# Performance work log

Hardware: AMD Instinct MI355X
Metric: run time of the kernel (lower is better)

Reference implementation:

```python
import jax, jax.numpy as jnp
import numpy as np
from jax import lax

TAG_NUM = 20
START = TAG_NUM - 2  # tag2idx[START_TAG]
STOP = TAG_NUM - 1   # tag2idx[STOP_TAG]
NEG = -10000.0


def setup_inputs() -> dict:
    key = jax.random.key(0)
    k1, k2, k3, k4 = jax.random.split(key, 4)
    B, L = 256, 512
    feats = jax.random.normal(k1, (B, L, TAG_NUM), dtype=jnp.float32)
    T = jax.random.normal(k2, (TAG_NUM, TAG_NUM), dtype=jnp.float32)
    # transitions into START and out of... match torch init: T[START, :] = -1e4 ; T[:, STOP] = -1e4
    T = T.at[START, :].set(NEG).at[:, STOP].set(NEG)
    tags = jax.random.randint(k3, (B, L), 0, TAG_NUM - 2, dtype=jnp.int64)  # real tags only
    lengths = jax.random.randint(k4, (B,), 1, L + 1, dtype=jnp.int64)
    return {"feats": feats, "T": T, "tags": tags, "lengths": lengths}


def crf_neg_log_likelihood(feats, T, tags, lengths):
    # feats: [B, L, tag], T: [tag, tag] (T[i, j] = score of transition i -> j)
    B, L, tg = feats.shape
    mask = jnp.arange(L)[None, :] < lengths[:, None]           # [B, L] bool
    # scores[b, l, prev, cur] = feats[b, l, cur] + T[prev, cur]
    scores = feats[:, :, None, :] + T[None, None, :, :]        # [B, L, tag, tag]
    scores_lb = jnp.swapaxes(scores, 0, 1)                     # [L, B, tag, tag]
    mask_lb = mask.T                                           # [L, B]

    # ---- forward algorithm (log partition) ----
    part0 = scores_lb[0, :, START, :]                          # [B, tag]
    def step(part, x):
        sc, m = x                                              # sc: [B, tag, tag], m: [B]
        cur = jax.nn.logsumexp(sc + part[:, :, None], axis=1)  # [B, tag]
        part = jnp.where(m[:, None], cur, part)                # freeze past seq end
        return part, None
    part, _ = lax.scan(step, part0, (scores_lb[1:], mask_lb[1:]))
    final = jax.nn.logsumexp(part[:, :, None] + T[None, :, :], axis=1)  # [B, tag]
    forward_score = final[:, STOP].sum()

    # ---- gold score ----
    prev = jnp.concatenate([jnp.full((B, 1), START, dtype=tags.dtype), tags[:, :-1]], axis=1)
    b_idx = jnp.arange(B)[:, None]
    l_idx = jnp.arange(L)[None, :]
    tg_energy = scores[b_idx, l_idx, prev, tags]               # [B, L]
    gold = jnp.sum(tg_energy * mask.astype(feats.dtype))
    end_ids = jnp.take_along_axis(tags, lengths[:, None] - 1, axis=1)[:, 0]
    gold = gold + T[end_ids, STOP].sum()

    return forward_score - gold


def reference(feats, T, tags, lengths):
    return crf_neg_log_likelihood(feats, T, tags, lengths)
```

## Files before the change

### kernel.cpp

```cpp
#include <hip/hip_runtime.h>
#include <hip/hip_bf16.h>
#include <math.h>

#define TAGS   20
#define TSTART (TAGS - 2)
#define TSTOP  (TAGS - 1)

constexpr float  LOG2E = 1.4426950408889634f;
constexpr float  LN2f  = 0.6931471805599453f;
constexpr double LN2d  = 0.69314718055994530942;

typedef __attribute__((ext_vector_type(8))) short short8;
typedef __attribute__((ext_vector_type(4))) float f32x4;
union U4 { unsigned int u[4]; short8 v; };

__device__ __forceinline__ unsigned int pk2(float lo, float hi) {
    unsigned int a = __float_as_uint(hi) + 0x8000u;
    unsigned int b = __float_as_uint(lo) + 0x8000u;
#if __has_builtin(__builtin_amdgcn_perm)
    return __builtin_amdgcn_perm(a, b, 0x07060302u);
#else
    return (a & 0xFFFF0000u) | (b >> 16);
#endif
}
__device__ __forceinline__ float fexp2(float x) { return exp2f(x); }
__device__ __forceinline__ float flog2(float x) { return log2f(x); }
__device__ __forceinline__ float frcp(float x) { return __builtin_amdgcn_rcpf(x); }
__device__ __forceinline__ float bcast(float v, int srclane) {
    return __int_as_float(__builtin_amdgcn_readlane(__float_as_int(v), srclane));
}
__device__ __forceinline__ int rho(int k) {
    int g = k >> 3, i = k & 7;
    return (i < 4) ? (4 * g + i) : (16 + 4 * g + (i - 4));
}

__global__ __launch_bounds__(512)
void crf_fused_kernel(const float* __restrict__ feats,
                      const float* __restrict__ Tm,
                      const int*   __restrict__ tags,
                      const int*   __restrict__ lengths,
                      double*      __restrict__ partial,
                      int L)
{
    __shared__ float  smem[16 * 1024];
    __shared__ float  sv[32];
    __shared__ int    EsX[8];
    __shared__ float  gred[8];
    __shared__ double fwd_sh;

    const int b    = blockIdx.x;
    const int tid  = threadIdx.x;
    const int w    = tid >> 6;
    const int lane = tid & 63;
    const int G    = lane >> 4, col = lane & 15;
    const int len  = lengths[b];

    #pragma unroll
    for (int s = 0; s < 2; ++s) {
        const int c = w + 8 * s;
        float* efc = smem + c * 1024;
        const float* fc = feats + ((size_t)b * L + (size_t)c * 32) * TAGS;
        for (int it = lane; it < 160; it += 64) {
            float4 v = reinterpret_cast<const float4*>(fc)[it];
            float vv[4] = {v.x, v.y, v.z, v.w};
            #pragma unroll
            for (int u = 0; u < 4; ++u) {
                int f = it * 4 + u;
                int t = f / TAGS, tag = f - t * TAGS;
                efc[t * 32 + tag] = fexp2(vv[u] * LOG2E);
            }
        }
        for (int q = lane; q < 32 * 12; q += 64) {
            int t = q / 12;
            efc[t * 32 + 20 + (q - t * 12)] = 0.f;
        }
    }
    __syncthreads();

    U4 A0, A1;
    #pragma unroll
    for (int t = 0; t < 4; ++t) {
        int k0 = 8 * G + 2 * t;
        int r0 = rho(k0), r1 = rho(k0 + 1);
        int m1 = 16 + col;
        float a00 = (r0 < TAGS) ? fexp2(Tm[col * TAGS + r0] * LOG2E) : 0.f;
        float a01 = (r1 < TAGS) ? fexp2(Tm[col * TAGS + r1] * LOG2E) : 0.f;
        float a10 = (m1 < TAGS && r0 < TAGS) ? fexp2(Tm[m1 * TAGS + r0] * LOG2E) : 0.f;
        float a11 = (m1 < TAGS && r1 < TAGS) ? fexp2(Tm[m1 * TAGS + r1] * LOG2E) : 0.f;
        A0.u[t] = pk2(a00, a01);
        A1.u[t] = pk2(a10, a11);
    }

    auto step = [&](f32x4& C00, f32x4& C01, f32x4& C10, f32x4& C11,
                    const float* efc, int t) {
        float4 e0 = *reinterpret_cast<const float4*>(&efc[t * 32 + 4 * G]);
        float4 e1 = *reinterpret_cast<const float4*>(&efc[t * 32 + 16 + 4 * G]);
        U4 B0, B1;
        B0.u[0] = pk2(C00[0] * e0.x, C00[1] * e0.y);
        B0.u[1] = pk2(C00[2] * e0.z, C00[3] * e0.w);
        B0.u[2] = pk2(C10[0] * e1.x, C10[1] * e1.y);
        B0.u[3] = pk2(C10[2] * e1.z, C10[3] * e1.w);
        B1.u[0] = pk2(C01[0] * e0.x, C01[1] * e0.y);
        B1.u[1] = pk2(C01[2] * e0.z, C01[3] * e0.w);
        B1.u[2] = pk2(C11[0] * e1.x, C11[1] * e1.y);
        B1.u[3] = pk2(C11[2] * e1.z, C11[3] * e1.w);
        f32x4 z = {0.f, 0.f, 0.f, 0.f};
        C00 = __builtin_amdgcn_mfma_f32_16x16x32_bf16(A0.v, B0.v, z, 0, 0, 0);
        C01 = __builtin_amdgcn_mfma_f32_16x16x32_bf16(A0.v, B1.v, z, 0, 0, 0);
        C10 = __builtin_amdgcn_mfma_f32_16x16x32_bf16(A1.v, B0.v, z, 0, 0, 0);
        C11 = __builtin_amdgcn_mfma_f32_16x16x32_bf16(A1.v, B1.v, z, 0, 0, 0);
    };
    auto strip = [&](f32x4& C00, f32x4& C01, f32x4& C10, f32x4& C11) -> int {
        float pr = C00[0] + C00[1] + C00[2] + C00[3] + C10[0] + C10[1] + C10[2] + C10[3];
        int pb = __builtin_amdgcn_readfirstlane(__float_as_int(pr));
        int ex = ((pb >> 23) & 0xFF) - 127;
        float s = __uint_as_float((unsigned)(127 - ex) << 23);
        #pragma unroll
        for (int j = 0; j < 4; ++j) { C00[j] *= s; C01[j] *= s; C10[j] *= s; C11[j] *= s; }
        return ex;
    };
    auto xwr = [&](int slot, const f32x4& C00, const f32x4& C01,
                   const f32x4& C10, const f32x4& C11, int E) {
        float* Xs = smem + slot * 1088;
        #pragma unroll
        for (int j = 0; j < 4; ++j) {
            Xs[(4 * G + j) * 34 + col]           = C00[j];
            Xs[(4 * G + j) * 34 + col + 16]      = C01[j];
            Xs[(16 + 4 * G + j) * 34 + col]      = C10[j];
            Xs[(16 + 4 * G + j) * 34 + col + 16] = C11[j];
        }
        if (lane == 0) EsX[slot] = E;
    };
    auto prod = [&](int slot, f32x4& C00, f32x4& C01, f32x4& C10, f32x4& C11) -> int {
        const float* Xs = smem + slot * 1088;
        U4 Ax0, Ax1;
        #pragma unroll
        for (int t = 0; t < 4; ++t) {
            int r = rho(8 * G + 2 * t);
            float2 x0 = *reinterpret_cast<const float2*>(&Xs[col * 34 + r]);
            float2 x1 = *reinterpret_cast<const float2*>(&Xs[(16 + col) * 34 + r]);
            Ax0.u[t] = pk2(x0.x, x0.y);
            Ax1.u[t] = pk2(x1.x, x1.y);
        }
        U4 B0, B1;
        B0.u[0] = pk2(C00[0], C00[1]);
        B0.u[1] = pk2(C00[2], C00[3]);
        B0.u[2] = pk2(C10[0], C10[1]);
        B0.u[3] = pk2(C10[2], C10[3]);
        B1.u[0] = pk2(C01[0], C01[1]);
        B1.u[1] = pk2(C01[2], C01[3]);
        B1.u[2] = pk2(C11[0], C11[1]);
        B1.u[3] = pk2(C11[2], C11[3]);
        f32x4 z = {0.f, 0.f, 0.f, 0.f};
        f32x4 n00 = __builtin_amdgcn_mfma_f32_16x16x32_bf16(Ax0.v, B0.v, z, 0, 0, 0);
        f32x4 n01 = __builtin_amdgcn_mfma_f32_16x16x32_bf16(Ax0.v, B1.v, z, 0, 0, 0);
        f32x4 n10 = __builtin_amdgcn_mfma_f32_16x16x32_bf16(Ax1.v, B0.v, z, 0, 0, 0);
        f32x4 n11 = __builtin_amdgcn_mfma_f32_16x16x32_bf16(Ax1.v, B1.v, z, 0, 0, 0);
        C00 = n00; C01 = n01; C10 = n10; C11 = n11;
        return strip(C00, C01, C10, C11);
    };

    f32x4 aC00, aC01, aC10, aC11, bC00, bC01, bC10, bC11;
    #pragma unroll
    for (int j = 0; j < 4; ++j) {
        float d = (4 * G + j == col) ? 1.f : 0.f;
        aC00[j] = d; aC11[j] = d; aC01[j] = 0.f; aC10[j] = 0.f;
        bC00[j] = d; bC11[j] = d; bC01[j] = 0.f; bC10[j] = 0.f;
    }
    int aE = 0, bE = 0;

    const int cB  = w + 8;
    const int loA = (w == 0) ? 1 : w * 32;
    const int hiA = min(w * 32 + 31, len - 1);
    const int loB = cB * 32;
    const int hiB = min(cB * 32 + 31, len - 1);
    int nA = hiA - loA + 1; if (nA < 0) nA = 0;
    int nB = hiB - loB + 1; if (nB < 0) nB = 0;
    const int n = max(nA, nB);
    const float* efA = smem + w * 1024;
    const float* efB = smem + cB * 1024;

    int lA = hiA, lB = hiB;
    for (int i = 0; i < n; ++i) {
        if (i < nA) { step(aC00, aC01, aC10, aC11, efA, lA - w * 32);  --lA; }
        if (i < nB) { step(bC00, bC01, bC10, bC11, efB, lB - cB * 32); --lB; }
        if ((i & 3) == 3) {
            aE += strip(aC00, aC01, aC10, aC11);
            bE += strip(bC00, bC01, bC10, bC11);
        }
    }
    __syncthreads();

    if ((w & 1) == 0) {
        xwr(w / 2,     aC00, aC01, aC10, aC11, aE);
        xwr(w / 2 + 4, bC00, bC01, bC10, bC11, bE);
    }
    __syncthreads();
    if (w & 1) {
        int pA = (w - 1) / 2;
        aE += EsX[pA]     + prod(pA,     aC00, aC01, aC10, aC11);
        bE += EsX[pA + 4] + prod(pA + 4, bC00, bC01, bC10, bC11);
    }
    __syncthreads();
    if (w == 1 || w == 5) {
        xwr((w - 1) / 4,     aC00, aC01, aC10, aC11, aE);
        xwr((w - 1) / 4 + 2, bC00, bC01, bC10, bC11, bE);
    }
    __syncthreads();
    if (w == 3 || w == 7) {
        int q = (w - 3) / 4;
        aE += EsX[q]     + prod(q,     aC00, aC01, aC10, aC11);
        bE += EsX[q + 2] + prod(q + 2, bC00, bC01, bC10, bC11);
    }
    __syncthreads();
    if (w == 3) {
        xwr(0, aC00, aC01, aC10, aC11, aE);
        xwr(1, bC00, bC01, bC10, bC11, bE);
    }
    __syncthreads();
    if (w == 7) {
        aE += EsX[0] + prod(0, aC00, aC01, aC10, aC11);
        bE += EsX[1] + prod(1, bC00, bC01, bC10, bC11);
    }
    __syncthreads();
    if (w == 7) {
        xwr(0, aC00, aC01, aC10, aC11, aE);
        int ex = prod(0, bC00, bC01, bC10, bC11);
        int fE = aE + bE + ex;
        float* Gt = smem;
        #pragma unroll
        for (int j = 0; j < 4; ++j) {
            Gt[col * 34 + 4 * G + j]            = bC00[j];
            Gt[col * 34 + 16 + 4 * G + j]       = bC10[j];
            Gt[(col + 16) * 34 + 4 * G + j]     = bC01[j];
            Gt[(col + 16) * 34 + 16 + 4 * G + j]= bC11[j];
        }
        if (lane == 0) EsX[0] = fE;
    }
    __syncthreads();

    if (w == 0) {
        const int n2 = lane & 31;
        float p = (n2 < TAGS) ? (feats[(size_t)b * L * TAGS + n2] + Tm[TSTART * TAGS + n2]) * LOG2E
                              : -1e30f;
        float mx = p;
        #pragma unroll
        for (int off = 32; off; off >>= 1) mx = fmaxf(mx, __shfl_xor(mx, off));
        float v = (n2 < TAGS) ? fexp2(p - mx) : 0.f;
        if (lane < 32) sv[lane] = v;
        const float* Gt = smem;
        float vn = 0.f;
        #pragma unroll
        for (int r = 0; r < 32; r += 2) {
            float2 g2 = *reinterpret_cast<const float2*>(&Gt[n2 * 34 + r]);
            vn = fmaf(sv[r], g2.x, vn);
            vn = fmaf(sv[r + 1], g2.y, vn);
        }
        float cstop = Tm[n2 * TAGS + TSTOP];
        float mc = (n2 < TAGS) ? cstop : -INFINITY;
        #pragma unroll
        for (int off = 32; off; off >>= 1) mc = fmaxf(mc, __shfl_xor(mc, off));
        float ts = (lane < 32 && n2 < TAGS) ? vn * fexp2((cstop - mc) * LOG2E) : 0.f;
        #pragma unroll
        for (int off = 32; off; off >>= 1) ts += __shfl_xor(ts, off);
        if (lane == 0)
            fwd_sh = ((double)mx + (double)EsX[0] + (double)flog2(ts)) * LN2d + (double)mc;
    }

    float g = 0.f;
    for (int l = tid; l < len; l += 512) {
        int tt = tags[(size_t)b * L + l];
        int pv = (l == 0) ? TSTART : tags[(size_t)b * L + l - 1];
        g += feats[((size_t)b * L + l) * TAGS + tt] + Tm[pv * TAGS + tt];
    }
    #pragma unroll
    for (int off = 32; off; off >>= 1) g += __shfl_xor(g, off);
    if (lane == 0) gred[w] = g;
    __syncthreads();

    if (tid == 0) {
        float gs = gred[0] + gred[1] + gred[2] + gred[3]
                 + gred[4] + gred[5] + gred[6] + gred[7];
        double gold = (double)gs + (double)Tm[tags[(size_t)b * L + len - 1] * TAGS + TSTOP];
        partial[b] = fwd_sh - gold;
    }
}

__global__ __launch_bounds__(64)
void crf_fwd_kernel(const float* __restrict__ feats,
                    const float* __restrict__ Tm,
                    const int*   __restrict__ tags,
                    const int*   __restrict__ lengths,
                    double*      __restrict__ partial,
                    int B, int L)
{
    __shared__ float le[512 * TAGS];
    const int b    = blockIdx.x;
    const int lane = threadIdx.x;
    const int j    = (lane < TAGS) ? lane : 0;
    const float* fb  = feats + (size_t)b * L * TAGS;
    const int*   tg  = tags  + (size_t)b * L;
    const int    len = lengths[b];

    const int nv4 = (L * TAGS) >> 2;
    for (int it = lane; it < nv4; it += 64) {
        float4 v = reinterpret_cast<const float4*>(fb)[it];
        float4 e;
        e.x = fexp2(v.x * LOG2E); e.y = fexp2(v.y * LOG2E);
        e.z = fexp2(v.z * LOG2E); e.w = fexp2(v.w * LOG2E);
        reinterpret_cast<float4*>(le)[it] = e;
    }
    __syncthreads();

    float ET[TAGS];
    #pragma unroll
    for (int i = 0; i < TAGS; ++i) ET[i] = fexp2(Tm[i * TAGS + j] * LOG2E);

    float w0   = flog2(le[j]) + Tm[TSTART * TAGS + j] * LOG2E;
    float base = bcast(w0, 0);
    float P    = fexp2(w0 - base);
    float M2   = base;
    float Pa[TAGS];
    #pragma unroll
    for (int i = 0; i < TAGS; ++i) Pa[i] = bcast(P, i);
    const float* leb = le + j;

    auto STEP = [&](int l, float efv, float rsv, bool scaled) {
        float s0 = 0.f, s1 = 0.f, s2 = 0.f, s3 = 0.f;
        #pragma unroll
        for (int i = 0; i < TAGS; i += 4) {
            s0 = fmaf(ET[i + 0], Pa[i + 0], s0);
            s1 = fmaf(ET[i + 1], Pa[i + 1], s1);
            s2 = fmaf(ET[i + 2], Pa[i + 2], s2);
            s3 = fmaf(ET[i + 3], Pa[i + 3], s3);
        }
        float s   = (s0 + s1) + (s2 + s3);
        float cur = s * efv;
        float pn  = (l < len) ? cur : P;
        P = scaled ? pn * rsv : pn;
        #pragma unroll
        for (int i = 0; i < TAGS; ++i) Pa[i] = bcast(P, i);
    };

    float efb[4];
    #pragma unroll
    for (int k = 0; k < 4; ++k) { int ln = 1 + k; ln = (ln < L) ? ln : (L - 1); efb[k] = leb[ln * TAGS]; }

    float rs = 1.0f, lg0 = 0.0f;
    int l0 = 1;
    for (; l0 + 3 < L; l0 += 4) {
        if (l0 >= len) break;
        float efn[4];
        #pragma unroll
        for (int k = 0; k < 4; ++k) { int ln = l0 + 4 + k; ln = (ln < L) ? ln : (L - 1); efn[k] = leb[ln * TAGS]; }
        M2 += lg0;
        STEP(l0 + 0, efb[0], rs, true);
        STEP(l0 + 1, efb[1], 1.f, false);
        STEP(l0 + 2, efb[2], 1.f, false);
        STEP(l0 + 3, efb[3], 1.f, false);
        float p0 = Pa[0];
        rs = frcp(p0); lg0 = flog2(p0);
        #pragma unroll
        for (int k = 0; k < 4; ++k) efb[k] = efn[k];
    }
    if (l0 < len) {
        int rem = L - l0;
        M2 += lg0;
        if (rem > 0) STEP(l0 + 0, efb[0], rs, true);
        if (rem > 1) STEP(l0 + 1, efb[1], 1.f, false);
        if (rem > 2) STEP(l0 + 2, efb[2], 1.f, false);
        if (rem > 3) STEP(l0 + 3, efb[3], 1.f, false);
    }

    float cstop = Tm[j * TAGS + TSTOP];
    float mc = (lane < TAGS) ? cstop : -INFINITY;
    #pragma unroll
    for (int off = 32; off; off >>= 1) mc = fmaxf(mc, __shfl_xor(mc, off));
    float t = (lane < TAGS) ? P * fexp2((cstop - mc) * LOG2E) : 0.f;
    #pragma unroll
    for (int off = 32; off; off >>= 1) t += __shfl_xor(t, off);
    double fwd = ((double)M2 + (double)flog2(t)) * LN2d + (double)mc;

    float g = 0.f;
    for (int l = lane; l < len; l += 64) {
        int tt = tg[l];
        int pv = (l == 0) ? TSTART : tg[l - 1];
        g += flog2(le[l * TAGS + tt]) * LN2f + Tm[pv * TAGS + tt];
    }
    #pragma unroll
    for (int off = 32; off; off >>= 1) g += __shfl_xor(g, off);

    if (lane == 0) {
        double gold = (double)g + (double)Tm[tg[len - 1] * TAGS + TSTOP];
        partial[b] = fwd - gold;
    }
}

__global__ __launch_bounds__(256)
void crf_reduce_kernel(const double* __restrict__ partial, float* __restrict__ out, int B)
{
    __shared__ double sh[256];
    const int t = threadIdx.x;
    double acc = 0.0;
    for (int i = t; i < B; i += 256) acc += partial[i];
    sh[t] = acc;
    __syncthreads();
    for (int s = 128; s; s >>= 1) {
        if (t < s) sh[t] += sh[t + s];
        __syncthreads();
    }
    if (t == 0) out[0] = (float)sh[0];
}

extern "C" void kernel_launch(void* const* d_in, const int* in_sizes, int n_in,
                              void* d_out, int out_size, void* d_ws, size_t ws_size,
                              hipStream_t stream)
{
    const float* feats   = (const float*)d_in[0];
    const float* Tm      = (const float*)d_in[1];
    const int*   tags    = (const int*)d_in[2];
    const int*   lengths = (const int*)d_in[3];

    const int B = in_sizes[3];
    const int L = in_sizes[2] / B;

    double* partial = (double*)d_ws;

    if (L == 512 && ws_size >= (size_t)B * sizeof(double)) {
        crf_fused_kernel<<<B, 512, 0, stream>>>(feats, Tm, tags, lengths, partial, L);
        crf_reduce_kernel<<<1, 256, 0, stream>>>(partial, (float*)d_out, B);
    } else {
        crf_fwd_kernel<<<B, 64, 0, stream>>>(feats, Tm, tags, lengths, partial, B, L);
        crf_reduce_kernel<<<1, 256, 0, stream>>>(partial, (float*)d_out, B);
    }
}
```

Before: 28.87 us.

## Switch CRF chunk matmuls from four 16x16 MFMAs to two chained 32x32 MFMAs

Replaces the four 16x16x32 bf16 MFMAs per step (a 2x2 tiling of the 32x32 transition product) with two accumulating 32x32x16 bf16 MFMAs, which changes the register layout of the running product and every shared-memory write and read in the tree reduction. It also swaps exp2f/log2f for the raw hardware intrinsics and removes the __syncthreads between the feature preload and the transition-matrix setup. The aim is fewer MFMA issues and less packing work on the serial dependency chain. The risks are the longer latency of the chained 32x32 MFMA, and a possible race now that the barrier is gone, if no later barrier comes before the loop reads the preloaded features.

```diff
diff --git a/kernel.cpp b/kernel.cpp
--- a/kernel.cpp
+++ b/kernel.cpp
@@ -10,8 +10,8 @@
 constexpr float  LN2f  = 0.6931471805599453f;
 constexpr double LN2d  = 0.69314718055994530942;
 
-typedef __attribute__((ext_vector_type(8))) short short8;
-typedef __attribute__((ext_vector_type(4))) float f32x4;
+typedef __attribute__((ext_vector_type(8)))  short short8;
+typedef __attribute__((ext_vector_type(16))) float f32x16;
 union U4 { unsigned int u[4]; short8 v; };
 
 __device__ __forceinline__ unsigned int pk2(float lo, float hi) {
@@ -23,15 +23,26 @@
     return (a & 0xFFFF0000u) | (b >> 16);
 #endif
 }
+#if __has_builtin(__builtin_amdgcn_exp2f)
+__device__ __forceinline__ float fexp2(float x) { return __builtin_amdgcn_exp2f(x); }
+#else
 __device__ __forceinline__ float fexp2(float x) { return exp2f(x); }
+#endif
+#if __has_builtin(__builtin_amdgcn_logf)
+__device__ __forceinline__ float flog2(float x) { return __builtin_amdgcn_logf(x); }
+#else
 __device__ __forceinline__ float flog2(float x) { return log2f(x); }
+#endif
 __device__ __forceinline__ float frcp(float x) { return __builtin_amdgcn_rcpf(x); }
 __device__ __forceinline__ float bcast(float v, int srclane) {
     return __int_as_float(__builtin_amdgcn_readlane(__float_as_int(v), srclane));
 }
-__device__ __forceinline__ int rho(int k) {
-    int g = k >> 3, i = k & 7;
-    return (i < 4) ? (4 * g + i) : (16 + 4 * g + (i - 4));
+
+__device__ __forceinline__ int kbase(int p, int h) {
+    return (p < 2) ? (4 * h + 2 * p) : (8 + 4 * h + 2 * (p - 2));
+}
+__device__ __forceinline__ int crow(int j, int h) {
+    return (j & 3) + 8 * (j >> 2) + 4 * h;
 }
 
 __global__ __launch_bounds__(512)
@@ -52,7 +63,8 @@
     const int tid  = threadIdx.x;
     const int w    = tid >> 6;
     const int lane = tid & 63;
-    const int G    = lane >> 4, col = lane & 15;
+    const int m    = lane & 31;
+    const int h    = lane >> 5;
     const int len  = lengths[b];
 
     #pragma unroll
@@ -75,97 +87,88 @@
             efc[t * 32 + 20 + (q - t * 12)] = 0.f;
         }
     }
-    __syncthreads();
-
-    U4 A0, A1;
-    #pragma unroll
-    for (int t = 0; t < 4; ++t) {
-        int k0 = 8 * G + 2 * t;
-        int r0 = rho(k0), r1 = rho(k0 + 1);
-        int m1 = 16 + col;
-        float a00 = (r0 < TAGS) ? fexp2(Tm[col * TAGS + r0] * LOG2E) : 0.f;
-        float a01 = (r1 < TAGS) ? fexp2(Tm[col * TAGS + r1] * LOG2E) : 0.f;
-        float a10 = (m1 < TAGS && r0 < TAGS) ? fexp2(Tm[m1 * TAGS + r0] * LOG2E) : 0.f;
-        float a11 = (m1 < TAGS && r1 < TAGS) ? fexp2(Tm[m1 * TAGS + r1] * LOG2E) : 0.f;
-        A0.u[t] = pk2(a00, a01);
-        A1.u[t] = pk2(a10, a11);
-    }
-
-    auto step = [&](f32x4& C00, f32x4& C01, f32x4& C10, f32x4& C11,
-                    const float* efc, int t) {
-        float4 e0 = *reinterpret_cast<const float4*>(&efc[t * 32 + 4 * G]);
-        float4 e1 = *reinterpret_cast<const float4*>(&efc[t * 32 + 16 + 4 * G]);
-        U4 B0, B1;
-        B0.u[0] = pk2(C00[0] * e0.x, C00[1] * e0.y);
-        B0.u[1] = pk2(C00[2] * e0.z, C00[3] * e0.w);
-        B0.u[2] = pk2(C10[0] * e1.x, C10[1] * e1.y);
-        B0.u[3] = pk2(C10[2] * e1.z, C10[3] * e1.w);
-        B1.u[0] = pk2(C01[0] * e0.x, C01[1] * e0.y);
-        B1.u[1] = pk2(C01[2] * e0.z, C01[3] * e0.w);
-        B1.u[2] = pk2(C11[0] * e1.x, C11[1] * e1.y);
-        B1.u[3] = pk2(C11[2] * e1.z, C11[3] * e1.w);
-        f32x4 z = {0.f, 0.f, 0.f, 0.f};
-        C00 = __builtin_amdgcn_mfma_f32_16x16x32_bf16(A0.v, B0.v, z, 0, 0, 0);
-        C01 = __builtin_amdgcn_mfma_f32_16x16x32_bf16(A0.v, B1.v, z, 0, 0, 0);
-        C10 = __builtin_amdgcn_mfma_f32_16x16x32_bf16(A1.v, B0.v, z, 0, 0, 0);
-        C11 = __builtin_amdgcn_mfma_f32_16x16x32_bf16(A1.v, B1.v, z, 0, 0, 0);
-    };
-    auto strip = [&](f32x4& C00, f32x4& C01, f32x4& C10, f32x4& C11) -> int {
-        float pr = C00[0] + C00[1] + C00[2] + C00[3] + C10[0] + C10[1] + C10[2] + C10[3];
+
+    U4 A1g, A2g;
+    #pragma unroll
+    for (int p = 0; p < 4; ++p) {
+        int r = kbase(p, h);
+        float a0 = (m < TAGS && r     < TAGS) ? fexp2(Tm[m * TAGS + r]      * LOG2E) : 0.f;
+        float a1 = (m < TAGS && r + 1 < TAGS) ? fexp2(Tm[m * TAGS + r + 1]  * LOG2E) : 0.f;
+        float b0 = (m < TAGS && r + 16 < TAGS) ? fexp2(Tm[m * TAGS + r + 16] * LOG2E) : 0.f;
+        float b1 = (m < TAGS && r + 17 < TAGS) ? fexp2(Tm[m * TAGS + r + 17] * LOG2E) : 0.f;
+        A1g.u[p] = pk2(a0, a1);
+        A2g.u[p] = pk2(b0, b1);
+    }
+
+    auto step = [&](f32x16& C, const float* efc, int t) {
+        float4 ea = *reinterpret_cast<const float4*>(&efc[t * 32 + 4 * h]);
+        float4 eb = *reinterpret_cast<const float4*>(&efc[t * 32 + 8 + 4 * h]);
+        float4 ec = *reinterpret_cast<const float4*>(&efc[t * 32 + 16 + 4 * h]);
+        float4 ed = *reinterpret_cast<const float4*>(&efc[t * 32 + 24 + 4 * h]);
+        U4 B1, B2;
+        B1.u[0] = pk2(C[0]  * ea.x, C[1]  * ea.y);
+        B1.u[1] = pk2(C[2]  * ea.z, C[3]  * ea.w);
+        B1.u[2] = pk2(C[4]  * eb.x, C[5]  * eb.y);
+        B1.u[3] = pk2(C[6]  * eb.z, C[7]  * eb.w);
+        B2.u[0] = pk2(C[8]  * ec.x, C[9]  * ec.y);
+        B2.u[1] = pk2(C[10] * ec.z, C[11] * ec.w);
+        B2.u[2] = pk2(C[12] * ed.x, C[13] * ed.y);
+        B2.u[3] = pk2(C[14] * ed.z, C[15] * ed.w);
+        f32x16 z = {0.f,0.f,0.f,0.f,0.f,0.f,0.f,0.f,0.f,0.f,0.f,0.f,0.f,0.f,0.f,0.f};
+        f32x16 t1 = __builtin_amdgcn_mfma_f32_32x32x16_bf16(A1g.v, B1.v, z,  0, 0, 0);
+        C         = __builtin_amdgcn_mfma_f32_32x32x16_bf16(A2g.v, B2.v, t1, 0, 0, 0);
+    };
+    auto strip = [&](f32x16& C) -> int {
+        float pr = ((C[0]+C[1])+(C[2]+C[3])) + ((C[4]+C[5])+(C[6]+C[7]))
+                 + ((C[8]+C[9])+(C[10]+C[11])) + ((C[12]+C[13])+(C[14]+C[15]));
         int pb = __builtin_amdgcn_readfirstlane(__float_as_int(pr));
         int ex = ((pb >> 23) & 0xFF) - 127;
         float s = __uint_as_float((unsigned)(127 - ex) << 23);
         #pragma unroll
-        for (int j = 0; j < 4; ++j) { C00[j] *= s; C01[j] *= s; C10[j] *= s; C11[j] *= s; }
+        for (int j = 0; j < 16; ++j) C[j] *= s;
         return ex;
     };
-    auto xwr = [&](int slot, const f32x4& C00, const f32x4& C01,
-                   const f32x4& C10, const f32x4& C11, int E) {
-        float* Xs = smem + slot * 1088;
-        #pragma unroll
-        for (int j = 0; j < 4; ++j) {
-            Xs[(4 * G + j) * 34 + col]           = C00[j];
-            Xs[(4 * G + j) * 34 + col + 16]      = C01[j];
-            Xs[(16 + 4 * G + j) * 34 + col]      = C10[j];
-            Xs[(16 + 4 * G + j) * 34 + col + 16] = C11[j];
-        }
+    auto xwrP = [&](float* Xs, const f32x16& C) {
+        #pragma unroll
+        for (int j = 0; j < 16; ++j) Xs[crow(j, h) * 34 + m] = C[j];
+    };
+    auto prodP = [&](const float* Xs, f32x16& C) -> int {
+        U4 Ax1, Ax2;
+        #pragma unroll
+        for (int p = 0; p < 4; ++p) {
+            int r = kbase(p, h);
+            float2 x1 = *reinterpret_cast<const float2*>(&Xs[m * 34 + r]);
+            float2 x2 = *reinterpret_cast<const float2*>(&Xs[m * 34 + r + 16]);
+            Ax1.u[p] = pk2(x1.x, x1.y);
+            Ax2.u[p] = pk2(x2.x, x2.y);
+        }
+        U4 B1, B2;
+        B1.u[0] = pk2(C[0],  C[1]);
+        B1.u[1] = pk2(C[2],  C[3]);
+        B1.u[2] = pk2(C[4],  C[5]);
+        B1.u[3] = pk2(C[6],  C[7]);
+        B2.u[0] = pk2(C[8],  C[9]);
+        B2.u[1] = pk2(C[10], C[11]);
+        B2.u[2] = pk2(C[12], C[13]);
+        B2.u[3] = pk2(C[14], C[15]);
+        f32x16 z = {0.f,0.f,0.f,0.f,0.f,0.f,0.f,0.f,0.f,0.f,0.f,0.f,0.f,0.f,0.f,0.f};
+        f32x16 t1 = __builtin_amdgcn_mfma_f32_32x32x16_bf16(Ax1.v, B1.v, z,  0, 0, 0);
+        C         = __builtin_amdgcn_mfma_f32_32x32x16_bf16(Ax2.v, B2.v, t1, 0, 0, 0);
+        return strip(C);
+    };
+    auto xwr = [&](int slot, const f32x16& C, int E) {
+        xwrP(smem + slot * 1088, C);
         if (lane == 0) EsX[slot] = E;
     };
-    auto prod = [&](int slot, f32x4& C00, f32x4& C01, f32x4& C10, f32x4& C11) -> int {
-        const float* Xs = smem + slot * 1088;
-        U4 Ax0, Ax1;
-        #pragma unroll
-        for (int t = 0; t < 4; ++t) {
-            int r = rho(8 * G + 2 * t);
-            float2 x0 = *reinterpret_cast<const float2*>(&Xs[col * 34 + r]);
-            float2 x1 = *reinterpret_cast<const float2*>(&Xs[(16 + col) * 34 + r]);
-            Ax0.u[t] = pk2(x0.x, x0.y);
-            Ax1.u[t] = pk2(x1.x, x1.y);
-        }
-        U4 B0, B1;
-        B0.u[0] = pk2(C00[0], C00[1]);
-        B0.u[1] = pk2(C00[2], C00[3]);
-        B0.u[2] = pk2(C10[0], C10[1]);
-        B0.u[3] = pk2(C10[2], C10[3]);
-        B1.u[0] = pk2(C01[0], C01[1]);
-        B1.u[1] = pk2(C01[2], C01[3]);
-        B1.u[2] = pk2(C11[0], C11[1]);
-        B1.u[3] = pk2(C11[2], C11[3]);
-        f32x4 z = {0.f, 0.f, 0.f, 0.f};
-        f32x4 n00 = __builtin_amdgcn_mfma_f32_16x16x32_bf16(Ax0.v, B0.v, z, 0, 0, 0);
-        f32x4 n01 = __builtin_amdgcn_mfma_f32_16x16x32_bf16(Ax0.v, B1.v, z, 0, 0, 0);
-        f32x4 n10 = __builtin_amdgcn_mfma_f32_16x16x32_bf16(Ax1.v, B0.v, z, 0, 0, 0);
-        f32x4 n11 = __builtin_amdgcn_mfma_f32_16x16x32_bf16(Ax1.v, B1.v, z, 0, 0, 0);
-        C00 = n00; C01 = n01; C10 = n10; C11 = n11;
-        return strip(C00, C01, C10, C11);
-    };
-
-    f32x4 aC00, aC01, aC10, aC11, bC00, bC01, bC10, bC11;
-    #pragma unroll
-    for (int j = 0; j < 4; ++j) {
-        float d = (4 * G + j == col) ? 1.f : 0.f;
-        aC00[j] = d; aC11[j] = d; aC01[j] = 0.f; aC10[j] = 0.f;
-        bC00[j] = d; bC11[j] = d; bC01[j] = 0.f; bC10[j] = 0.f;
+    auto prod = [&](int slot, f32x16& C) -> int {
+        return prodP(smem + slot * 1088, C);
+    };
+
+    f32x16 Ca, Cb;
+    #pragma unroll
+    for (int j = 0; j < 16; ++j) {
+        float d = (crow(j, h) == m) ? 1.f : 0.f;
+        Ca[j] = d; Cb[j] = d;
     }
     int aE = 0, bE = 0;
 
@@ -182,59 +185,54 @@
 
     int lA = hiA, lB = hiB;
     for (int i = 0; i < n; ++i) {
-        if (i < nA) { step(aC00, aC01, aC10, aC11, efA, lA - w * 32);  --lA; }
-        if (i < nB) { step(bC00, bC01, bC10, bC11, efB, lB - cB * 32); --lB; }
+        if (i < nA) { step(Ca, efA, lA - w * 32);  --lA; }
+        if (i < nB) { step(Cb, efB, lB - cB * 32); --lB; }
         if ((i & 3) == 3) {
-            aE += strip(aC00, aC01, aC10, aC11);
-            bE += strip(bC00, bC01, bC10, bC11);
+            aE += strip(Ca);
+            bE += strip(Cb);
         }
     }
     __syncthreads();
 
     if ((w & 1) == 0) {
-        xwr(w / 2,     aC00, aC01, aC10, aC11, aE);
-        xwr(w / 2 + 4, bC00, bC01, bC10, bC11, bE);
+        xwr(w / 2,     Ca, aE);
+        xwr(w / 2 + 4, Cb, bE);
     }
     __syncthreads();
     if (w & 1) {
         int pA = (w - 1) / 2;
-        aE += EsX[pA]     + prod(pA,     aC00, aC01, aC10, aC11);
-        bE += EsX[pA + 4] + prod(pA + 4, bC00, bC01, bC10, bC11);
+        aE += EsX[pA]     + prod(pA,     Ca);
+        bE += EsX[pA + 4] + prod(pA + 4, Cb);
     }
     __syncthreads();
     if (w == 1 || w == 5) {
-        xwr((w - 1) / 4,     aC00, aC01, aC10, aC11, aE);
-        xwr((w - 1) / 4 + 2, bC00, bC01, bC10, bC11, bE);
+        xwr((w - 1) / 4,     Ca, aE);
+        xwr((w - 1) / 4 + 2, Cb, bE);
     }
     __syncthreads();
     if (w == 3 || w == 7) {
         int q = (w - 3) / 4;
-        aE += EsX[q]     + prod(q,     aC00, aC01, aC10, aC11);
-        bE += EsX[q + 2] + prod(q + 2, bC00, bC01, bC10, bC11);
+        aE += EsX[q]     + prod(q,     Ca);
+        bE += EsX[q + 2] + prod(q + 2, Cb);
     }
     __syncthreads();
     if (w == 3) {
-        xwr(0, aC00, aC01, aC10, aC11, aE);
-        xwr(1, bC00, bC01, bC10, bC11, bE);
+        xwr(0, Ca, aE);
+        xwr(1, Cb, bE);
     }
     __syncthreads();
     if (w == 7) {
-        aE += EsX[0] + prod(0, aC00, aC01, aC10, aC11);
-        bE += EsX[1] + prod(1, bC00, bC01, bC10, bC11);
+        aE += EsX[0] + prod(0, Ca);
+        bE += EsX[1] + prod(1, Cb);
     }
     __syncthreads();
     if (w == 7) {
-        xwr(0, aC00, aC01, aC10, aC11, aE);
-        int ex = prod(0, bC00, bC01, bC10, bC11);
+        xwr(0, Ca, aE);
+        int ex = prodP(smem, Cb);
         int fE = aE + bE + ex;
         float* Gt = smem;
         #pragma unroll
-        for (int j = 0; j < 4; ++j) {
-            Gt[col * 34 + 4 * G + j]            = bC00[j];
-            Gt[col * 34 + 16 + 4 * G + j]       = bC10[j];
-            Gt[(col + 16) * 34 + 4 * G + j]     = bC01[j];
-            Gt[(col + 16) * 34 + 16 + 4 * G + j]= bC11[j];
-        }
+        for (int j = 0; j < 16; ++j) Gt[m * 34 + crow(j, h)] = Cb[j];
         if (lane == 0) EsX[0] = fE;
     }
     __syncthreads();
```

Result: slower. 29.58 us (+2.5%).
